# Kernel optimization log

Measured on AMD Instinct MI355X. Metric: run time of the kernel, lower is better.

Reference implementation:

```python
import jax, jax.numpy as jnp
import numpy as np

B, S, D, N, HD, M = 2, 2048, 1024, 16, 64, 4096  # batch, seq, d_model, heads, head_dim, d_mlp


def setup_inputs() -> dict:
    key = jax.random.key(0)
    ks = jax.random.split(key, 8)
    sd = 1.0 / np.sqrt(D)
    return {
        "x": jax.random.normal(ks[0], (B, S, D), dtype=jnp.float32),
        "W_qkv": jax.random.normal(ks[1], (N, D, 3 * HD), dtype=jnp.float32) * sd,
        "W_out": jax.random.normal(ks[2], (N, HD, D), dtype=jnp.float32) * sd,
        "ln1_w": jnp.ones((D,), jnp.float32),
        "ln1_b": jnp.zeros((D,), jnp.float32),
        "ln2_w": jnp.ones((D,), jnp.float32),
        "ln2_b": jnp.zeros((D,), jnp.float32),
        "W1": jax.random.normal(ks[3], (D, M), dtype=jnp.float32) * sd,
        "b1": jnp.zeros((M,), jnp.float32),
        "W2": jax.random.normal(ks[4], (M, D), dtype=jnp.float32) / np.sqrt(M),
        "b2": jnp.zeros((D,), jnp.float32),
    }


def _layernorm(x, w, b, eps=1e-4):
    mu = jnp.mean(x, axis=-1, keepdims=True)
    var = jnp.var(x, axis=-1, keepdims=True, ddof=1)  # torch unbiased var
    return w * (x - mu) / jnp.sqrt(var + eps) + b


def _attention(x, W_qkv, W_out):
    b, s, d = x.shape
    qkv = jnp.einsum('bsd,ndh->bnsh', x, W_qkv)  # [b,n,s,3*hd]
    q, k, v = jnp.split(qkv, 3, axis=-1)
    hd = q.shape[-1]
    attn = jnp.einsum('bnqh,bnkh->bnqk', q, k) / np.sqrt(hd)
    mask = -1e10 * (1.0 - jnp.tril(jnp.ones((s, s), jnp.float32)))
    attn = jax.nn.softmax(attn + mask, axis=-1)
    out = jnp.einsum('bnqk,bnkh->bnqh', attn, v)  # [b,n,s,hd]
    # faithful to torch: raw memory reinterpretation (b,n,s,hd) -> (b, n*hd, s)
    out = out.reshape(b, -1, s)
    # faithful to torch: d is a shared free index -> W_out summed over (n,h)
    out = jnp.einsum('bds,nhd->bsd', out, W_out)
    return out


def _mlp(x, W1, b1, W2, b2):
    h = jax.nn.gelu(x @ W1 + b1, approximate=False)
    return h @ W2 + b2


def reference(x, W_qkv, W_out, ln1_w, ln1_b, ln2_w, ln2_b, W1, b1, W2, b2):
    x = x + _attention(_layernorm(x, ln1_w, ln1_b), W_qkv, W_out)
    x = x + _mlp(_layernorm(x, ln2_w, ln2_b), W1, b1, W2, b2)
    return x
```

## Files before the change

### kernel.cpp

```cpp
#include <hip/hip_runtime.h>

typedef unsigned short ushort_t;
typedef __attribute__((ext_vector_type(8))) short short8;
typedef __attribute__((ext_vector_type(4))) float floatx4;
typedef __attribute__((ext_vector_type(4))) unsigned short ushort4v;

#define B_ 2
#define S_ 2048
#define D_ 1024
#define NH_ 16
#define HD_ 64
#define M_ 4096

#define KSCALE 0.18033688011112042f

__device__ __forceinline__ ushort_t f2bf(float f) {
    unsigned u = __builtin_bit_cast(unsigned, f);
    return (ushort_t)((u + 0x7FFFu + ((u >> 16) & 1u)) >> 16);
}

__device__ __forceinline__ void gload_lds16(const ushort_t* g, ushort_t* l) {
    __builtin_amdgcn_global_load_lds(
        (const __attribute__((address_space(1))) unsigned int*)(g),
        (__attribute__((address_space(3))) unsigned int*)(l), 16, 0, 0);
}

__device__ __forceinline__ void transpose64(
    const float* __restrict__ src, ushort_t* __restrict__ dst,
    int srs, int drs, int by, int bx, int tid, ushort_t (*tileT)[68]) {
    const int tx = tid & 15, ty = tid >> 4;
    const int c0 = bx * 64 + tx * 4;
    #pragma unroll
    for (int i = 0; i < 4; ++i) {
        int r = by * 64 + ty + i * 16;
        float4 v = *(const float4*)(src + (size_t)r * srs + c0);
        int rl = ty + i * 16;
        tileT[tx * 4 + 0][rl] = f2bf(v.x);
        tileT[tx * 4 + 1][rl] = f2bf(v.y);
        tileT[tx * 4 + 2][rl] = f2bf(v.z);
        tileT[tx * 4 + 3][rl] = f2bf(v.w);
    }
    __syncthreads();
    #pragma unroll
    for (int i = 0; i < 4; ++i) {
        int cc = ty + i * 16;
        int rr = tx * 4;
        *(ushort4v*)(dst + (size_t)(bx * 64 + cc) * drs + by * 64 + rr) =
            *(const ushort4v*)&tileT[cc][rr];
    }
}

__global__ __launch_bounds__(256) void prep_kernel(
    const float* __restrict__ W_qkv, const float* __restrict__ W1,
    const float* __restrict__ W2, const float* __restrict__ W_out,
    ushort_t* __restrict__ WqkvT, ushort_t* __restrict__ W1T,
    ushort_t* __restrict__ W2T, float* __restrict__ wsum) {
    __shared__ ushort_t tileT[64][68];
    const int bid = blockIdx.x;
    const int tid = threadIdx.x;
    if (bid < 768) {
        int bz = bid / 48, rem = bid % 48;
        int by = rem / 3, bx = rem % 3;
        transpose64(W_qkv + (size_t)bz * D_ * 192, WqkvT + (size_t)bz * 192 * D_,
                    192, D_, by, bx, tid, tileT);
    } else if (bid < 768 + 1024) {
        int r = bid - 768;
        transpose64(W1, W1T, M_, D_, r / 64, r % 64, tid, tileT);
    } else if (bid < 768 + 2048) {
        int r = bid - 1792;
        transpose64(W2, W2T, D_, M_, r / 16, r % 16, tid, tileT);
    } else {
        int cb = bid - 2816;
        float* part = (float*)tileT;
        int tx = tid & 31;
        int col = cb * 32 + tx;
        int rg = tid >> 5;
        float s = 0.f;
        for (int r = rg; r < NH_ * HD_; r += 8) s += W_out[(size_t)r * D_ + col];
        part[tid] = s;
        __syncthreads();
        if (tid < 32) {
            float t = 0.f;
            #pragma unroll
            for (int g = 0; g < 8; ++g) t += part[g * 32 + tid];
            wsum[cb * 32 + tid] = t;
        }
    }
}

__global__ __launch_bounds__(256) void ln1_kernel(const float* __restrict__ x,
                                                  const float* __restrict__ w,
                                                  const float* __restrict__ b,
                                                  ushort_t* __restrict__ out) {
    int row = blockIdx.x, tid = threadIdx.x;
    float v[4], s = 0.f, ss = 0.f;
    #pragma unroll
    for (int i = 0; i < 4; ++i) {
        v[i] = x[(size_t)row * D_ + tid + i * 256];
        s += v[i]; ss += v[i] * v[i];
    }
    #pragma unroll
    for (int off = 32; off >= 1; off >>= 1) { s += __shfl_xor(s, off); ss += __shfl_xor(ss, off); }
    __shared__ float red[8];
    if ((tid & 63) == 0) { red[(tid >> 6) * 2] = s; red[(tid >> 6) * 2 + 1] = ss; }
    __syncthreads();
    s = red[0] + red[2] + red[4] + red[6];
    ss = red[1] + red[3] + red[5] + red[7];
    float mu = s * (1.f / D_);
    float var = (ss - (float)D_ * mu * mu) * (1.f / (D_ - 1));
    float rstd = rsqrtf(var + 1e-4f);
    #pragma unroll
    for (int i = 0; i < 4; ++i) {
        int d = tid + i * 256;
        out[(size_t)row * D_ + d] = f2bf((v[i] - mu) * rstd * w[d] + b[d]);
    }
}

__global__ __launch_bounds__(256) void gather_resid(
    const float* __restrict__ x, const float* __restrict__ attn,
    const float* __restrict__ wsum, float* __restrict__ x1) {
    __shared__ float tile[128][65];
    const int tid = threadIdx.x;
    const int dchunk = blockIdx.x;
    const int stile = blockIdx.y;
    const int b = stile >> 5, shi = stile & 31;
    const int h = tid & 63;
    const int wv = tid >> 6;
    #pragma unroll
    for (int r = 0; r < 32; ++r) {
        int dloc = r * 4 + wv;
        int d = dchunk * 128 + dloc;
        int q = ((d & 63) << 5) + shi;
        tile[dloc][h] = attn[((size_t)(b * NH_ + (d >> 6)) * S_ + q) * HD_ + h];
    }
    __syncthreads();
    const int row0 = b * S_ + shi * 64;
    #pragma unroll
    for (int r = 0; r < 32; ++r) {
        int sr = r * 2 + (tid >> 7);
        int dcol = tid & 127;
        int d = dchunk * 128 + dcol;
        size_t idx = (size_t)(row0 + sr) * D_ + d;
        x1[idx] = x[idx] + wsum[d] * tile[dcol][sr];
    }
}

template <int EPI>
__global__ __launch_bounds__(256) void gemm_bt(
    const ushort_t* __restrict__ A, const ushort_t* __restrict__ BT,
    int M, int N, int K, int ld, const float* __restrict__ bias,
    const float* __restrict__ resid, void* __restrict__ outp, void* __restrict__ outp2) {
    __shared__ __align__(16) ushort_t As[128 * 64];
    __shared__ __align__(16) ushort_t Bs[128 * 64];
    const int tid = threadIdx.x;
    const int lane = tid & 63, wave = tid >> 6;
    const int ln15 = lane & 15, qd = lane >> 4;
    const int wm = wave >> 1, wn = wave & 1;
    const int bm = blockIdx.y, bn = blockIdx.x;
    const int lr = lane >> 3;
    const int sw = (lane & 7) ^ lr;
    if (EPI == 3) {
        A += (size_t)blockIdx.z * K;
        BT += (size_t)blockIdx.z * K;
    }

    floatx4 acc[4][4];
    #pragma unroll
    for (int i = 0; i < 4; ++i)
        #pragma unroll
        for (int j = 0; j < 4; ++j) acc[i][j] = (floatx4){0.f, 0.f, 0.f, 0.f};

    for (int k0 = 0; k0 < K; k0 += 64) {
        __syncthreads();
        #pragma unroll
        for (int l = 0; l < 4; ++l) {
            int r0 = (l * 4 + wave) * 8;
            gload_lds16(A + (size_t)(bm * 128 + r0 + lr) * ld + k0 + sw * 8, &As[r0 * 64]);
            gload_lds16(BT + (size_t)(bn * 128 + r0 + lr) * ld + k0 + sw * 8, &Bs[r0 * 64]);
        }
        __syncthreads();
        #pragma unroll
        for (int ks = 0; ks < 2; ++ks) {
            short8 a[4], b[4];
            #pragma unroll
            for (int mt = 0; mt < 4; ++mt) {
                int row = wm * 64 + mt * 16 + ln15;
                a[mt] = *(const short8*)&As[row * 64 + (((ks * 4 + qd) ^ (row & 7)) << 3)];
            }
            #pragma unroll
            for (int nt = 0; nt < 4; ++nt) {
                int row = wn * 64 + nt * 16 + ln15;
                b[nt] = *(const short8*)&Bs[row * 64 + (((ks * 4 + qd) ^ (row & 7)) << 3)];
            }
            #pragma unroll
            for (int mt = 0; mt < 4; ++mt)
                #pragma unroll
                for (int nt = 0; nt < 4; ++nt)
                    acc[mt][nt] = __builtin_amdgcn_mfma_f32_16x16x32_bf16(a[mt], b[nt], acc[mt][nt], 0, 0, 0);
        }
    }

    const int row0 = bm * 128 + wm * 64, col0 = bn * 128 + wn * 64;
    #pragma unroll
    for (int mt = 0; mt < 4; ++mt)
        #pragma unroll
        for (int nt = 0; nt < 4; ++nt) {
            if (EPI == 0) {
                int col = col0 + nt * 16 + ln15;
                unsigned uc = (unsigned)col;
                unsigned hn = uc / 192u;
                unsigned j = uc - hn * 192u;
                int rowb = row0 + mt * 16 + qd * 4;
                int bb = rowb >> 11, sidx = rowb & 2047;
                if (j < 128u) {
                    #pragma unroll
                    for (int r = 0; r < 4; ++r) {
                        float v = acc[mt][nt][r];
                        if (j >= 64u) v *= KSCALE;
                        ((ushort_t*)outp)[(((size_t)bb * NH_ + hn) * S_ + sidx + r) * 192 + j] = f2bf(v);
                    }
                } else {
                    ushort4v pk;
                    #pragma unroll
                    for (int r = 0; r < 4; ++r) pk[r] = f2bf(acc[mt][nt][r]);
                    *(ushort4v*)&((ushort_t*)outp2)[((size_t)(bb * NH_ + hn) * HD_ + (j - 128u)) * S_ + sidx] = pk;
                }
            } else {
                #pragma unroll
                for (int r = 0; r < 4; ++r) {
                    int row = row0 + mt * 16 + qd * 4 + r;
                    int col = col0 + nt * 16 + ln15;
                    float v = acc[mt][nt][r];
                    if (EPI == 1) {
                        v += bias[col];
                        float u = v * (0.7978845608f + 0.0356774081f * v * v);
                        float e = exp2f(fminf(u * 2.88539008f, 80.f));
                        float rc = __builtin_amdgcn_rcpf(e + 1.f);
                        float g = v * (1.f - rc);
                        ((ushort_t*)outp)[(size_t)row * N + col] = f2bf(g);
                    } else if (EPI == 2) {
                        v += bias[col] + resid[(size_t)row * N + col];
                        ((float*)outp)[(size_t)row * N + col] = v;
                    } else {
                        float* po = (float*)outp + (size_t)blockIdx.z * M * N;
                        po[(size_t)row * N + col] = v;
                    }
                }
            }
        }
}

__global__ __launch_bounds__(256) void mlp2_reduce(const float* __restrict__ part,
                                                   const float* __restrict__ b2,
                                                   const float* __restrict__ x1,
                                                   float* __restrict__ out) {
    const size_t NTOT = (size_t)B_ * S_ * D_;
    size_t i = ((size_t)blockIdx.x * 256 + threadIdx.x) * 4;
    floatx4 s = *(const floatx4*)(part + i);
    s += *(const floatx4*)(part + NTOT + i);
    s += *(const floatx4*)(part + 2 * NTOT + i);
    s += *(const floatx4*)(part + 3 * NTOT + i);
    int col = (int)(i & (D_ - 1));
    s += *(const floatx4*)(b2 + col);
    s += *(const floatx4*)(x1 + i);
    *(floatx4*)(out + i) = s;
}

__global__ __launch_bounds__(256) void attn_kernel(const ushort_t* __restrict__ qkv,
                                                   const ushort_t* __restrict__ vT,
                                                   float* __restrict__ attn_out) {
    __shared__ __align__(16) ushort_t Ks[128 * 64];
    __shared__ __align__(16) ushort_t Vs[64 * 128];
    __shared__ __align__(16) ushort_t Ps[4][16 * 72];
    const int tid = threadIdx.x, lane = tid & 63, w = tid >> 6;
    const int ln15 = lane & 15, qd = lane >> 4;
    const int qt = (int)gridDim.x - 1 - (int)blockIdx.x;
    const int bh = blockIdx.z * NH_ + blockIdx.y;
    const int qb = qt * 64 + w * 16;
    const size_t qbase = (size_t)bh * S_ * 192;
    const size_t vtbase = (size_t)bh * HD_ * S_;
    ushort_t* myP = (ushort_t*)Ps[w];

    const ushort_t* qrow = qkv + qbase + (size_t)(qb + ln15) * 192;
    short8 bq[2];
    bq[0] = *(const short8*)(qrow + qd * 8);
    bq[1] = *(const short8*)(qrow + 32 + qd * 8);

    float lcur = 0.f;
    floatx4 oacc[4];
    #pragma unroll
    for (int mt = 0; mt < 4; ++mt) oacc[mt] = (floatx4){0.f, 0.f, 0.f, 0.f};

    auto qk_half = [&](int kh, floatx4* s) {
        #pragma unroll
        for (int mt = 0; mt < 4; ++mt) s[mt] = (floatx4){0.f, 0.f, 0.f, 0.f};
        #pragma unroll
        for (int ks = 0; ks < 2; ++ks)
            #pragma unroll
            for (int mt = 0; mt < 4; ++mt) {
                int row = kh * 64 + mt * 16 + ln15;
                short8 ak = *(const short8*)&Ks[row * 64 + (((ks * 4 + qd) ^ (row & 7)) << 3)];
                s[mt] = __builtin_amdgcn_mfma_f32_16x16x32_bf16(ak, bq[ks], s[mt], 0, 0, 0);
            }
    };
    auto softmax_pv = [&](floatx4* s, int kh, bool mask) {
        if (mask) {
            int q = qb + ln15;
            #pragma unroll
            for (int mt = 0; mt < 4; ++mt)
                #pragma unroll
                for (int r = 0; r < 4; ++r)
                    if (qt * 64 + mt * 16 + qd * 4 + r > q) s[mt][r] = -1e30f;
        }
        float rsum = 0.f;
        #pragma unroll
        for (int mt = 0; mt < 4; ++mt) {
            ushort4v pk;
            #pragma unroll
            for (int r = 0; r < 4; ++r) {
                float p = exp2f(s[mt][r]);
                rsum += p;
                pk[r] = (ushort_t)(__builtin_bit_cast(unsigned, p) >> 16);
            }
            *(ushort4v*)&myP[ln15 * 72 + mt * 16 + qd * 4] = pk;
        }
        rsum += __shfl_xor(rsum, 16);
        rsum += __shfl_xor(rsum, 32);
        lcur += rsum;
        #pragma unroll
        for (int g2 = 0; g2 < 2; ++g2) {
            short8 bp = *(const short8*)&myP[ln15 * 72 + g2 * 32 + qd * 8];
            #pragma unroll
            for (int mt = 0; mt < 4; ++mt) {
                int row = mt * 16 + ln15;
                short8 av = *(const short8*)&Vs[row * 128 + (((kh * 8 + g2 * 4 + qd) ^ (row & 15)) << 3)];
                oacc[mt] = __builtin_amdgcn_mfma_f32_16x16x32_bf16(av, bp, oacc[mt], 0, 0, 0);
            }
        }
    };

    const int ntiles = qt + 1;
    for (int kt2 = 0; kt2 < ntiles; kt2 += 2) {
        __syncthreads();
        #pragma unroll
        for (int i = 0; i < 4; ++i) {
            int gb = (i * 4 + w) * 64;
            int g = gb + lane;
            int krow = g >> 3;
            int kcg = (g & 7) ^ (krow & 7);
            int key = kt2 * 64 + krow; if (key > S_ - 1) key = S_ - 1;
            gload_lds16(qkv + qbase + (size_t)key * 192 + 64 + kcg * 8, &Ks[gb * 8]);
            int vrow = g >> 4;
            int vcg = (g & 15) ^ (vrow & 15);
            int vkey = kt2 * 64 + vcg * 8; if (vkey > S_ - 8) vkey = S_ - 8;
            gload_lds16(vT + vtbase + (size_t)vrow * S_ + vkey, &Vs[gb * 8]);
        }
        __syncthreads();

        if (kt2 + 1 < ntiles) {
            floatx4 s0[4], s1[4];
            qk_half(0, s0);
            qk_half(1, s1);
            softmax_pv(s0, 0, false);
            softmax_pv(s1, 1, kt2 + 1 == qt);
        } else {
            floatx4 s0[4];
            qk_half(0, s0);
            softmax_pv(s0, 0, kt2 == qt);
        }
    }
    float inv = 1.f / lcur;
    int q = qb + ln15;
    #pragma unroll
    for (int mt = 0; mt < 4; ++mt) {
        floatx4 o = oacc[mt] * inv;
        *(floatx4*)&attn_out[((size_t)bh * S_ + q) * HD_ + mt * 16 + qd * 4] = o;
    }
}

extern "C" void kernel_launch(void* const* d_in, const int* in_sizes, int n_in,
                              void* d_out, int out_size, void* d_ws, size_t ws_size,
                              hipStream_t stream) {
    const float* x = (const float*)d_in[0];
    const float* W_qkv = (const float*)d_in[1];
    const float* W_out = (const float*)d_in[2];
    const float* ln1_w = (const float*)d_in[3];
    const float* ln1_b = (const float*)d_in[4];
    const float* ln2_w = (const float*)d_in[5];
    const float* ln2_b = (const float*)d_in[6];
    const float* W1 = (const float*)d_in[7];
    const float* b1 = (const float*)d_in[8];
    const float* W2 = (const float*)d_in[9];
    const float* b2 = (const float*)d_in[10];

    char* ws = (char*)d_ws;
    const size_t MB = 1024 * 1024;
    ushort_t* ln1_out = (ushort_t*)(ws + 0 * MB);
    ushort_t* WqkvT   = (ushort_t*)(ws + 8 * MB);
    ushort_t* qkv     = (ushort_t*)(ws + 14 * MB);
    ushort_t* vT      = (ushort_t*)(ws + 38 * MB);
    float*    attn_o  = (float*)(ws + 46 * MB);
    float*    partials = (float*)(ws + 0 * MB);
    float*    x1      = (float*)(ws + 64 * MB);
    ushort_t* ln2_out = (ushort_t*)(ws + 80 * MB);
    ushort_t* W1T     = (ushort_t*)(ws + 88 * MB);
    ushort_t* hbuf    = (ushort_t*)(ws + 96 * MB);
    ushort_t* W2T     = (ushort_t*)(ws + 128 * MB);
    float*    wsum    = (float*)(ws + 136 * MB);

    prep_kernel<<<dim3(2848), 256, 0, stream>>>(W_qkv, W1, W2, W_out, WqkvT, W1T, W2T, wsum);
    ln1_kernel<<<dim3(B_ * S_), 256, 0, stream>>>(x, ln1_w, ln1_b, ln1_out);
    gemm_bt<0><<<dim3(3072 / 128, (B_ * S_) / 128), 256, 0, stream>>>(
        ln1_out, WqkvT, B_ * S_, 3072, D_, D_, nullptr, nullptr, qkv, vT);
    attn_kernel<<<dim3(S_ / 64, NH_, B_), 256, 0, stream>>>(qkv, vT, attn_o);
    gather_resid<<<dim3(8, 64), 256, 0, stream>>>(x, attn_o, wsum, x1);
    ln1_kernel<<<dim3(B_ * S_), 256, 0, stream>>>(x1, ln2_w, ln2_b, ln2_out);
    gemm_bt<1><<<dim3(M_ / 128, (B_ * S_) / 128), 256, 0, stream>>>(
        ln2_out, W1T, B_ * S_, M_, D_, D_, b1, nullptr, hbuf, nullptr);
    gemm_bt<3><<<dim3(D_ / 128, (B_ * S_) / 128, 4), 256, 0, stream>>>(
        hbuf, W2T, B_ * S_, D_, M_ / 4, M_, nullptr, nullptr, partials, nullptr);
    mlp2_reduce<<<dim3((B_ * S_ * D_) / 1024), 256, 0, stream>>>(partials, b2, x1, (float*)d_out);
}
```

Baseline: 424.6 us.

## Fuse LN1 into prep, atomic split-K for MLP2, pair causal attention tiles

Folds the first layernorm into the weight-prep launch as extra blocks. The attention residual kernel now also writes x1+b2 directly into the output, so the split-K MLP2 GEMM can atomically add its partials there, removing the partials buffer and the reduce kernel. The attention kernel now has each block process two query tiles, a long one and a short one, to balance causal work and halve the grid. Atomic float adds make the summation order nondeterministic and add atomic traffic on the output.

```diff
diff --git a/kernel.cpp b/kernel.cpp
--- a/kernel.cpp
+++ b/kernel.cpp
@@ -50,11 +50,38 @@
     }
 }
 
+__device__ __forceinline__ void ln_body(const float* __restrict__ x, const float* __restrict__ w,
+                                        const float* __restrict__ b, ushort_t* __restrict__ out,
+                                        int row, int tid, float* red) {
+    float v[4], s = 0.f, ss = 0.f;
+    #pragma unroll
+    for (int i = 0; i < 4; ++i) {
+        v[i] = x[(size_t)row * D_ + tid + i * 256];
+        s += v[i]; ss += v[i] * v[i];
+    }
+    #pragma unroll
+    for (int off = 32; off >= 1; off >>= 1) { s += __shfl_xor(s, off); ss += __shfl_xor(ss, off); }
+    if ((tid & 63) == 0) { red[(tid >> 6) * 2] = s; red[(tid >> 6) * 2 + 1] = ss; }
+    __syncthreads();
+    s = red[0] + red[2] + red[4] + red[6];
+    ss = red[1] + red[3] + red[5] + red[7];
+    float mu = s * (1.f / D_);
+    float var = (ss - (float)D_ * mu * mu) * (1.f / (D_ - 1));
+    float rstd = rsqrtf(var + 1e-4f);
+    #pragma unroll
+    for (int i = 0; i < 4; ++i) {
+        int d = tid + i * 256;
+        out[(size_t)row * D_ + d] = f2bf((v[i] - mu) * rstd * w[d] + b[d]);
+    }
+}
+
 __global__ __launch_bounds__(256) void prep_kernel(
     const float* __restrict__ W_qkv, const float* __restrict__ W1,
     const float* __restrict__ W2, const float* __restrict__ W_out,
     ushort_t* __restrict__ WqkvT, ushort_t* __restrict__ W1T,
-    ushort_t* __restrict__ W2T, float* __restrict__ wsum) {
+    ushort_t* __restrict__ W2T, float* __restrict__ wsum,
+    const float* __restrict__ x, const float* __restrict__ ln1_w,
+    const float* __restrict__ ln1_b, ushort_t* __restrict__ ln1_out) {
     __shared__ ushort_t tileT[64][68];
     const int bid = blockIdx.x;
     const int tid = threadIdx.x;
@@ -69,7 +96,7 @@
     } else if (bid < 768 + 2048) {
         int r = bid - 1792;
         transpose64(W2, W2T, D_, M_, r / 16, r % 16, tid, tileT);
-    } else {
+    } else if (bid < 2848) {
         int cb = bid - 2816;
         float* part = (float*)tileT;
         int tx = tid & 31;
@@ -85,6 +112,8 @@
             for (int g = 0; g < 8; ++g) t += part[g * 32 + tid];
             wsum[cb * 32 + tid] = t;
         }
+    } else {
+        ln_body(x, ln1_w, ln1_b, ln1_out, bid - 2848, tid, (float*)tileT);
     }
 }
 
@@ -92,33 +121,14 @@
                                                   const float* __restrict__ w,
                                                   const float* __restrict__ b,
                                                   ushort_t* __restrict__ out) {
-    int row = blockIdx.x, tid = threadIdx.x;
-    float v[4], s = 0.f, ss = 0.f;
-    #pragma unroll
-    for (int i = 0; i < 4; ++i) {
-        v[i] = x[(size_t)row * D_ + tid + i * 256];
-        s += v[i]; ss += v[i] * v[i];
-    }
-    #pragma unroll
-    for (int off = 32; off >= 1; off >>= 1) { s += __shfl_xor(s, off); ss += __shfl_xor(ss, off); }
     __shared__ float red[8];
-    if ((tid & 63) == 0) { red[(tid >> 6) * 2] = s; red[(tid >> 6) * 2 + 1] = ss; }
-    __syncthreads();
-    s = red[0] + red[2] + red[4] + red[6];
-    ss = red[1] + red[3] + red[5] + red[7];
-    float mu = s * (1.f / D_);
-    float var = (ss - (float)D_ * mu * mu) * (1.f / (D_ - 1));
-    float rstd = rsqrtf(var + 1e-4f);
-    #pragma unroll
-    for (int i = 0; i < 4; ++i) {
-        int d = tid + i * 256;
-        out[(size_t)row * D_ + d] = f2bf((v[i] - mu) * rstd * w[d] + b[d]);
-    }
+    ln_body(x, w, b, out, blockIdx.x, threadIdx.x, red);
 }
 
 __global__ __launch_bounds__(256) void gather_resid(
     const float* __restrict__ x, const float* __restrict__ attn,
-    const float* __restrict__ wsum, float* __restrict__ x1) {
+    const float* __restrict__ wsum, const float* __restrict__ b2,
+    float* __restrict__ x1, float* __restrict__ outd) {
     __shared__ float tile[128][65];
     const int tid = threadIdx.x;
     const int dchunk = blockIdx.x;
@@ -135,13 +145,17 @@
     }
     __syncthreads();
     const int row0 = b * S_ + shi * 64;
+    const int dcol = tid & 127;
+    const int d = dchunk * 128 + dcol;
+    const float wsd = wsum[d];
+    const float b2d = b2[d];
     #pragma unroll
     for (int r = 0; r < 32; ++r) {
         int sr = r * 2 + (tid >> 7);
-        int dcol = tid & 127;
-        int d = dchunk * 128 + dcol;
         size_t idx = (size_t)(row0 + sr) * D_ + d;
-        x1[idx] = x[idx] + wsum[d] * tile[dcol][sr];
+        float val = x[idx] + wsd * tile[dcol][sr];
+        x1[idx] = val;
+        outd[idx] = val + b2d;
     }
 }
 
@@ -149,7 +163,7 @@
 __global__ __launch_bounds__(256) void gemm_bt(
     const ushort_t* __restrict__ A, const ushort_t* __restrict__ BT,
     int M, int N, int K, int ld, const float* __restrict__ bias,
-    const float* __restrict__ resid, void* __restrict__ outp, void* __restrict__ outp2) {
+    void* __restrict__ outp, void* __restrict__ outp2) {
     __shared__ __align__(16) ushort_t As[128 * 64];
     __shared__ __align__(16) ushort_t Bs[128 * 64];
     const int tid = threadIdx.x;
@@ -159,7 +173,7 @@
     const int bm = blockIdx.y, bn = blockIdx.x;
     const int lr = lane >> 3;
     const int sw = (lane & 7) ^ lr;
-    if (EPI == 3) {
+    if (EPI == 4) {
         A += (size_t)blockIdx.z * K;
         BT += (size_t)blockIdx.z * K;
     }
@@ -238,32 +252,12 @@
                         float rc = __builtin_amdgcn_rcpf(e + 1.f);
                         float g = v * (1.f - rc);
                         ((ushort_t*)outp)[(size_t)row * N + col] = f2bf(g);
-                    } else if (EPI == 2) {
-                        v += bias[col] + resid[(size_t)row * N + col];
-                        ((float*)outp)[(size_t)row * N + col] = v;
                     } else {
-                        float* po = (float*)outp + (size_t)blockIdx.z * M * N;
-                        po[(size_t)row * N + col] = v;
+                        unsafeAtomicAdd((float*)outp + (size_t)row * N + col, v);
                     }
                 }
             }
         }
-}
-
-__global__ __launch_bounds__(256) void mlp2_reduce(const float* __restrict__ part,
-                                                   const float* __restrict__ b2,
-                                                   const float* __restrict__ x1,
-                                                   float* __restrict__ out) {
-    const size_t NTOT = (size_t)B_ * S_ * D_;
-    size_t i = ((size_t)blockIdx.x * 256 + threadIdx.x) * 4;
-    floatx4 s = *(const floatx4*)(part + i);
-    s += *(const floatx4*)(part + NTOT + i);
-    s += *(const floatx4*)(part + 2 * NTOT + i);
-    s += *(const floatx4*)(part + 3 * NTOT + i);
-    int col = (int)(i & (D_ - 1));
-    s += *(const floatx4*)(b2 + col);
-    s += *(const floatx4*)(x1 + i);
-    *(floatx4*)(out + i) = s;
 }
 
 __global__ __launch_bounds__(256) void attn_kernel(const ushort_t* __restrict__ qkv,
@@ -274,107 +268,112 @@
     __shared__ __align__(16) ushort_t Ps[4][16 * 72];
     const int tid = threadIdx.x, lane = tid & 63, w = tid >> 6;
     const int ln15 = lane & 15, qd = lane >> 4;
-    const int qt = (int)gridDim.x - 1 - (int)blockIdx.x;
+    const int px = blockIdx.x;
     const int bh = blockIdx.z * NH_ + blockIdx.y;
-    const int qb = qt * 64 + w * 16;
     const size_t qbase = (size_t)bh * S_ * 192;
     const size_t vtbase = (size_t)bh * HD_ * S_;
     ushort_t* myP = (ushort_t*)Ps[w];
 
-    const ushort_t* qrow = qkv + qbase + (size_t)(qb + ln15) * 192;
-    short8 bq[2];
-    bq[0] = *(const short8*)(qrow + qd * 8);
-    bq[1] = *(const short8*)(qrow + 32 + qd * 8);
-
-    float lcur = 0.f;
-    floatx4 oacc[4];
-    #pragma unroll
-    for (int mt = 0; mt < 4; ++mt) oacc[mt] = (floatx4){0.f, 0.f, 0.f, 0.f};
-
-    auto qk_half = [&](int kh, floatx4* s) {
-        #pragma unroll
-        for (int mt = 0; mt < 4; ++mt) s[mt] = (floatx4){0.f, 0.f, 0.f, 0.f};
-        #pragma unroll
-        for (int ks = 0; ks < 2; ++ks)
+    #pragma unroll 1
+    for (int pq = 0; pq < 2; ++pq) {
+        const int qt = pq ? px : 31 - px;
+        const int qb = qt * 64 + w * 16;
+
+        const ushort_t* qrow = qkv + qbase + (size_t)(qb + ln15) * 192;
+        short8 bq[2];
+        bq[0] = *(const short8*)(qrow + qd * 8);
+        bq[1] = *(const short8*)(qrow + 32 + qd * 8);
+
+        float lcur = 0.f;
+        floatx4 oacc[4];
+        #pragma unroll
+        for (int mt = 0; mt < 4; ++mt) oacc[mt] = (floatx4){0.f, 0.f, 0.f, 0.f};
+
+        auto qk_half = [&](int kh, floatx4* s) {
+            #pragma unroll
+            for (int mt = 0; mt < 4; ++mt) s[mt] = (floatx4){0.f, 0.f, 0.f, 0.f};
+            #pragma unroll
+            for (int ks = 0; ks < 2; ++ks)
+                #pragma unroll
+                for (int mt = 0; mt < 4; ++mt) {
+                    int row = kh * 64 + mt * 16 + ln15;
+                    short8 ak = *(const short8*)&Ks[row * 64 + (((ks * 4 + qd) ^ (row & 7)) << 3)];
+                    s[mt] = __builtin_amdgcn_mfma_f32_16x16x32_bf16(ak, bq[ks], s[mt], 0, 0, 0);
+                }
+        };
+        auto softmax_pv = [&](floatx4* s, int kh, bool mask) {
+            if (mask) {
+                int q = qb + ln15;
+                #pragma unroll
+                for (int mt = 0; mt < 4; ++mt)
+                    #pragma unroll
+                    for (int r = 0; r < 4; ++r)
+                        if (qt * 64 + mt * 16 + qd * 4 + r > q) s[mt][r] = -1e30f;
+            }
+            float rsum = 0.f;
             #pragma unroll
             for (int mt = 0; mt < 4; ++mt) {
-                int row = kh * 64 + mt * 16 + ln15;
-                short8 ak = *(const short8*)&Ks[row * 64 + (((ks * 4 + qd) ^ (row & 7)) << 3)];
-                s[mt] = __builtin_amdgcn_mfma_f32_16x16x32_bf16(ak, bq[ks], s[mt], 0, 0, 0);
-            }
-    };
-    auto softmax_pv = [&](floatx4* s, int kh, bool mask) {
-        if (mask) {
-            int q = qb + ln15;
-            #pragma unroll
-            for (int mt = 0; mt < 4; ++mt)
-                #pragma unroll
-                for (int r = 0; r < 4; ++r)
-                    if (qt * 64 + mt * 16 + qd * 4 + r > q) s[mt][r] = -1e30f;
-        }
-        float rsum = 0.f;
+                ushort4v pk;
+                #pragma unroll
+                for (int r = 0; r < 4; ++r) {
+                    float p = exp2f(s[mt][r]);
+                    rsum += p;
+                    pk[r] = (ushort_t)(__builtin_bit_cast(unsigned, p) >> 16);
+                }
+                *(ushort4v*)&myP[ln15 * 72 + mt * 16 + qd * 4] = pk;
+            }
+            rsum += __shfl_xor(rsum, 16);
+            rsum += __shfl_xor(rsum, 32);
+            lcur += rsum;
+            #pragma unroll
+            for (int g2 = 0; g2 < 2; ++g2) {
+                short8 bp = *(const short8*)&myP[ln15 * 72 + g2 * 32 + qd * 8];
+                #pragma unroll
+                for (int mt = 0; mt < 4; ++mt) {
+                    int row = mt * 16 + ln15;
+                    short8 av = *(const short8*)&Vs[row * 128 + (((kh * 8 + g2 * 4 + qd) ^ (row & 15)) << 3)];
+                    oacc[mt] = __builtin_amdgcn_mfma_f32_16x16x32_bf16(av, bp, oacc[mt], 0, 0, 0);
+                }
+            }
+        };
+
+        const int ntiles = qt + 1;
+        for (int kt2 = 0; kt2 < ntiles; kt2 += 2) {
+            __syncthreads();
+            #pragma unroll
+            for (int i = 0; i < 4; ++i) {
+                int gb = (i * 4 + w) * 64;
+                int g = gb + lane;
+                int krow = g >> 3;
+                int kcg = (g & 7) ^ (krow & 7);
+                int key = kt2 * 64 + krow; if (key > S_ - 1) key = S_ - 1;
+                gload_lds16(qkv + qbase + (size_t)key * 192 + 64 + kcg * 8, &Ks[gb * 8]);
+                int vrow = g >> 4;
+                int vcg = (g & 15) ^ (vrow & 15);
+                int vkey = kt2 * 64 + vcg * 8; if (vkey > S_ - 8) vkey = S_ - 8;
+                gload_lds16(vT + vtbase + (size_t)vrow * S_ + vkey, &Vs[gb * 8]);
+            }
+            __syncthreads();
+
+            if (kt2 + 1 < ntiles) {
+                floatx4 s0[4], s1[4];
+                qk_half(0, s0);
+                qk_half(1, s1);
+                softmax_pv(s0, 0, false);
+                softmax_pv(s1, 1, kt2 + 1 == qt);
+            } else {
+                floatx4 s0[4];
+                qk_half(0, s0);
+                softmax_pv(s0, 0, kt2 == qt);
+            }
+        }
+        float inv = 1.f / lcur;
+        int q = qb + ln15;
         #pragma unroll
         for (int mt = 0; mt < 4; ++mt) {
-            ushort4v pk;
-            #pragma unroll
-            for (int r = 0; r < 4; ++r) {
-                float p = exp2f(s[mt][r]);
-                rsum += p;
-                pk[r] = (ushort_t)(__builtin_bit_cast(unsigned, p) >> 16);
-            }
-            *(ushort4v*)&myP[ln15 * 72 + mt * 16 + qd * 4] = pk;
-        }
-        rsum += __shfl_xor(rsum, 16);
-        rsum += __shfl_xor(rsum, 32);
-        lcur += rsum;
-        #pragma unroll
-        for (int g2 = 0; g2 < 2; ++g2) {
-            short8 bp = *(const short8*)&myP[ln15 * 72 + g2 * 32 + qd * 8];
-            #pragma unroll
-            for (int mt = 0; mt < 4; ++mt) {
-                int row = mt * 16 + ln15;
-                short8 av = *(const short8*)&Vs[row * 128 + (((kh * 8 + g2 * 4 + qd) ^ (row & 15)) << 3)];
-                oacc[mt] = __builtin_amdgcn_mfma_f32_16x16x32_bf16(av, bp, oacc[mt], 0, 0, 0);
-            }
-        }
-    };
-
-    const int ntiles = qt + 1;
-    for (int kt2 = 0; kt2 < ntiles; kt2 += 2) {
-        __syncthreads();
-        #pragma unroll
-        for (int i = 0; i < 4; ++i) {
-            int gb = (i * 4 + w) * 64;
-            int g = gb + lane;
-            int krow = g >> 3;
-            int kcg = (g & 7) ^ (krow & 7);
-            int key = kt2 * 64 + krow; if (key > S_ - 1) key = S_ - 1;
-            gload_lds16(qkv + qbase + (size_t)key * 192 + 64 + kcg * 8, &Ks[gb * 8]);
-            int vrow = g >> 4;
-            int vcg = (g & 15) ^ (vrow & 15);
-            int vkey = kt2 * 64 + vcg * 8; if (vkey > S_ - 8) vkey = S_ - 8;
-            gload_lds16(vT + vtbase + (size_t)vrow * S_ + vkey, &Vs[gb * 8]);
-        }
-        __syncthreads();
-
-        if (kt2 + 1 < ntiles) {
-            floatx4 s0[4], s1[4];
-            qk_half(0, s0);
-            qk_half(1, s1);
-            softmax_pv(s0, 0, false);
-            softmax_pv(s1, 1, kt2 + 1 == qt);
-        } else {
-            floatx4 s0[4];
-            qk_half(0, s0);
-            softmax_pv(s0, 0, kt2 == qt);
-        }
-    }
-    float inv = 1.f / lcur;
-    int q = qb + ln15;
-    #pragma unroll
-    for (int mt = 0; mt < 4; ++mt) {
-        floatx4 o = oacc[mt] * inv;
-        *(floatx4*)&attn_out[((size_t)bh * S_ + q) * HD_ + mt * 16 + qd * 4] = o;
+            floatx4 o = oacc[mt] * inv;
+            *(floatx4*)&attn_out[((size_t)bh * S_ + q) * HD_ + mt * 16 + qd * 4] = o;
+        }
     }
 }
 
@@ -400,7 +399,6 @@
     ushort_t* qkv     = (ushort_t*)(ws + 14 * MB);
     ushort_t* vT      = (ushort_t*)(ws + 38 * MB);
     float*    attn_o  = (float*)(ws + 46 * MB);
-    float*    partials = (float*)(ws + 0 * MB);
     float*    x1      = (float*)(ws + 64 * MB);
     ushort_t* ln2_out = (ushort_t*)(ws + 80 * MB);
     ushort_t* W1T     = (ushort_t*)(ws + 88 * MB);
@@ -408,16 +406,15 @@
     ushort_t* W2T     = (ushort_t*)(ws + 128 * MB);
     float*    wsum    = (float*)(ws + 136 * MB);
 
-    prep_kernel<<<dim3(2848), 256, 0, stream>>>(W_qkv, W1, W2, W_out, WqkvT, W1T, W2T, wsum);
-    ln1_kernel<<<dim3(B_ * S_), 256, 0, stream>>>(x, ln1_w, ln1_b, ln1_out);
+    prep_kernel<<<dim3(2848 + B_ * S_), 256, 0, stream>>>(
+        W_qkv, W1, W2, W_out, WqkvT, W1T, W2T, wsum, x, ln1_w, ln1_b, ln1_out);
     gemm_bt<0><<<dim3(3072 / 128, (B_ * S_) / 128), 256, 0, stream>>>(
-        ln1_out, WqkvT, B_ * S_, 3072, D_, D_, nullptr, nullptr, qkv, vT);
-    attn_kernel<<<dim3(S_ / 64, NH_, B_), 256, 0, stream>>>(qkv, vT, attn_o);
-    gather_resid<<<dim3(8, 64), 256, 0, stream>>>(x, attn_o, wsum, x1);
+        ln1_out, WqkvT, B_ * S_, 3072, D_, D_, nullptr, qkv, vT);
+    attn_kernel<<<dim3(S_ / 128, NH_, B_), 256, 0, stream>>>(qkv, vT, attn_o);
+    gather_resid<<<dim3(8, 64), 256, 0, stream>>>(x, attn_o, wsum, b2, x1, (float*)d_out);
     ln1_kernel<<<dim3(B_ * S_), 256, 0, stream>>>(x1, ln2_w, ln2_b, ln2_out);
     gemm_bt<1><<<dim3(M_ / 128, (B_ * S_) / 128), 256, 0, stream>>>(
-        ln2_out, W1T, B_ * S_, M_, D_, D_, b1, nullptr, hbuf, nullptr);
-    gemm_bt<3><<<dim3(D_ / 128, (B_ * S_) / 128, 4), 256, 0, stream>>>(
-        hbuf, W2T, B_ * S_, D_, M_ / 4, M_, nullptr, nullptr, partials, nullptr);
-    mlp2_reduce<<<dim3((B_ * S_ * D_) / 1024), 256, 0, stream>>>(partials, b2, x1, (float*)d_out);
-}
+        ln2_out, W1T, B_ * S_, M_, D_, D_, b1, hbuf, nullptr);
+    gemm_bt<4><<<dim3(D_ / 128, (B_ * S_) / 128, 4), 256, 0, stream>>>(
+        hbuf, W2T, B_ * S_, D_, M_ / 4, M_, nullptr, (float*)d_out, nullptr);
+}
```

New measurement: 413.6 us. -2.6%, faster.
